# Kernel tuning notes

Hardware: AMD Instinct MI355X
Metric: run time of the kernel (lower is better)

## Reference

```python
import jax, jax.numpy as jnp
import numpy as np

N, L, D_MODEL, NUM_HEADS, MAX_SEQ = 4, 1024, 1024, 16, 2048
DEPTH = D_MODEL // NUM_HEADS


def setup_inputs() -> dict:
    key = jax.random.key(0)
    ks = jax.random.split(key, 12)
    inv = 1.0 / np.sqrt(D_MODEL)
    inp = {
        "q_in": jax.random.normal(ks[0], (N, L, D_MODEL), jnp.float32),
        "k_in": jax.random.normal(ks[1], (N, L, D_MODEL), jnp.float32),
        "v_in": jax.random.normal(ks[2], (N, L, D_MODEL), jnp.float32),
        # causal additive mask: 1.0 where attention is disallowed (j > i)
        "mask": (jnp.triu(jnp.ones((L, L), jnp.float32), k=1))[None, None, :, :],
        "Wq": jax.random.normal(ks[3], (D_MODEL, D_MODEL), jnp.float32) * inv,
        "bq": jnp.zeros((D_MODEL,), jnp.float32),
        "Wk": jax.random.normal(ks[4], (D_MODEL, D_MODEL), jnp.float32) * inv,
        "bk": jnp.zeros((D_MODEL,), jnp.float32),
        "Wv": jax.random.normal(ks[5], (D_MODEL, D_MODEL), jnp.float32) * inv,
        "bv": jnp.zeros((D_MODEL,), jnp.float32),
        "Wo": jax.random.normal(ks[6], (D_MODEL, D_MODEL), jnp.float32) * inv,
        "bo": jnp.zeros((D_MODEL,), jnp.float32),
        "pos_emb": jax.random.normal(ks[7], (MAX_SEQ, DEPTH), jnp.float32) * 0.02,
    }
    return inp


def _rel_bias(q, pos_emb):
    """q: [N,H,L,depth] -> skewed relative-position bias s: [N,H,L,L]."""
    n, h, l, d = q.shape
    e = pos_emb[pos_emb.shape[0] - l:, :]                     # [L, depth]
    qe = jnp.einsum('nhld,md->nhlm', q, e)                    # [N,H,L,L]
    # keep only the last (i+1) entries of row i (upper-left triangle zeroed)
    m = qe.shape[-1]
    keep = (jnp.arange(m)[None, :] >= (m - 1 - jnp.arange(l))[:, None]).astype(qe.dtype)
    qe = qe * keep
    # skew via pad/reshape/slice
    padded = jnp.pad(qe, ((0, 0), (0, 0), (0, 0), (1, 0)))    # [N,H,L,L+1]
    s = padded.reshape(n, h, l + 1, l)[:, :, 1:, :]           # [N,H,L,L]
    return s


def reference(q_in, k_in, v_in, mask, Wq, bq, Wk, bk, Wv, bv, Wo, bo, pos_emb):
    n, l, dm = q_in.shape
    h, d = NUM_HEADS, DEPTH

    def split(x):
        return x.reshape(n, l, h, d).transpose(0, 2, 1, 3)    # [N,H,L,depth]

    q = split(q_in @ Wq + bq)
    k = split(k_in @ Wk + bk)
    v = split(v_in @ Wv + bv)

    s = _rel_bias(q, pos_emb)
    logits = (jnp.einsum('nhld,nhmd->nhlm', q, k) + s) / jnp.sqrt(jnp.float32(d))
    logits = logits + mask * (-1e9)
    attn = jax.nn.softmax(logits, axis=-1)                    # [N,H,L,L]
    out = jnp.einsum('nhlm,nhmd->nhld', attn, v)
    out = out.transpose(0, 2, 1, 3).reshape(n, l, dm)
    return out @ Wo + bo
```

## Files before the change

kernel.cpp:

```cpp
#include <hip/hip_runtime.h>

typedef unsigned short u16t;
typedef unsigned int   u32t;
typedef __bf16 bf16x8 __attribute__((ext_vector_type(8)));
typedef float  f32x4  __attribute__((ext_vector_type(4)));

#define NB     4
#define SEQ    1024
#define DMODEL 1024
#define NHEAD  16
#define DEPTH  64
#define MAXSEQ 2048
#define MTOK   (NB * SEQ)

#define AS1 __attribute__((address_space(1)))
#define AS3 __attribute__((address_space(3)))

__device__ __forceinline__ u16t f2bf(float f) {
  u32t u = __builtin_bit_cast(u32t, f);
  u32t r = (u + 0x7fffu + ((u >> 16) & 1u)) >> 16;
  return (u16t)r;
}
__device__ __forceinline__ float bf2f(u16t h) {
  return __builtin_bit_cast(float, (u32t)h << 16);
}
__device__ __forceinline__ void load_lds16(const void* g, void* l) {
  __builtin_amdgcn_global_load_lds((AS1 u32t*)(g), (AS3 u32t*)(l), 16, 0, 0);
}
__device__ __forceinline__ bf16x8 pack8(f32x4 a, f32x4 b) {
  bf16x8 r;
  r[0] = (__bf16)a[0]; r[1] = (__bf16)a[1]; r[2] = (__bf16)a[2]; r[3] = (__bf16)a[3];
  r[4] = (__bf16)b[0]; r[5] = (__bf16)b[1]; r[6] = (__bf16)b[2]; r[7] = (__bf16)b[3];
  return r;
}

__global__ void transpose4_kernel(const float* __restrict__ w0, const float* __restrict__ w1,
                                  const float* __restrict__ w2, const float* __restrict__ w3,
                                  u16t* __restrict__ t0, u16t* __restrict__ t1,
                                  u16t* __restrict__ t2, u16t* __restrict__ t3,
                                  const float* __restrict__ pe, u16t* __restrict__ Er) {
  const int z = blockIdx.z;
  if (z == 4) {
    const int flat = blockIdx.y * 32 + blockIdx.x;
    if (flat < 256) {
      const int idx = flat * 256 + threadIdx.x;
      const int r = idx >> 6, d = idx & 63;
      Er[idx] = f2bf(pe[(size_t)(MAXSEQ - 1 - r) * DEPTH + d]);
    }
    return;
  }
  const float* W = (z == 0) ? w0 : ((z == 1) ? w1 : ((z == 2) ? w2 : w3));
  u16t* WT = (z == 0) ? t0 : ((z == 1) ? t1 : ((z == 2) ? t2 : t3));
  __shared__ float tile[32][33];
  const int tx = threadIdx.x & 31, ty = threadIdx.x >> 5;
  const int bx = blockIdx.x * 32, by = blockIdx.y * 32;
#pragma unroll
  for (int r = 0; r < 32; r += 8)
    tile[ty + r][tx] = W[(size_t)(by + ty + r) * DMODEL + bx + tx];
  __syncthreads();
#pragma unroll
  for (int r = 0; r < 32; r += 8)
    WT[(size_t)(bx + ty + r) * DMODEL + by + tx] = f2bf(tile[tx][ty + r]);
}

__device__ __forceinline__ void gemm_qkv_body(
    const float* __restrict__ A32, const u16t* __restrict__ BT,
    const float* __restrict__ bias, u16t* __restrict__ C,
    int M, int Nc, int K, int bx, int by, float scale) {
  __shared__ __align__(16) u16t As[128 * 32];
  __shared__ __align__(16) u16t Bs[128 * 32];
  const int tid = threadIdx.x;
  const int wave = tid >> 6;
  const int lane = tid & 63;
  const int q = lane >> 4, t = lane & 15;
  const int lrow = lane >> 2, lch = lane & 3;
  const int bm = by * 128, bn = bx * 128;
  const int wi = (wave >> 1) * 64, wj = (wave & 1) * 64;

  f32x4 acc[4][4];
#pragma unroll
  for (int i = 0; i < 4; ++i)
#pragma unroll
    for (int j = 0; j < 4; ++j) acc[i][j] = f32x4{0.f, 0.f, 0.f, 0.f};

  for (int kt = 0; kt < K; kt += 32) {
    __syncthreads();
    {
      const int rb0 = wave * 16, rb1 = 64 + wave * 16;
      const u16t* gb0 = BT + (size_t)(bn + rb0 + lrow) * K + kt + lch * 8;
      const u16t* gb1 = BT + (size_t)(bn + rb1 + lrow) * K + kt + lch * 8;
      load_lds16(gb0, Bs + rb0 * 32);
      load_lds16(gb1, Bs + rb1 * 32);
      const float* ga0 = A32 + (size_t)(bm + rb0 + lrow) * K + kt + lch * 8;
      const float* ga1 = A32 + (size_t)(bm + rb1 + lrow) * K + kt + lch * 8;
      f32x4 a00 = *(const f32x4*)ga0, a01 = *(const f32x4*)(ga0 + 4);
      f32x4 a10 = *(const f32x4*)ga1, a11 = *(const f32x4*)(ga1 + 4);
      *(bf16x8*)(As + (rb0 + lrow) * 32 + lch * 8) = pack8(a00, a01);
      *(bf16x8*)(As + (rb1 + lrow) * 32 + lch * 8) = pack8(a10, a11);
    }
    __syncthreads();
    bf16x8 af[4], bfr[4];
#pragma unroll
    for (int i = 0; i < 4; ++i) {
      af[i]  = *(const bf16x8*)(As + (wi + i * 16 + t) * 32 + q * 8);
      bfr[i] = *(const bf16x8*)(Bs + (wj + i * 16 + t) * 32 + q * 8);
    }
#pragma unroll
    for (int i = 0; i < 4; ++i)
#pragma unroll
      for (int j = 0; j < 4; ++j)
        acc[i][j] = __builtin_amdgcn_mfma_f32_16x16x32_bf16(af[i], bfr[j], acc[i][j], 0, 0, 0);
  }
#pragma unroll
  for (int j = 0; j < 4; ++j) {
    const int col = bn + wj + j * 16 + t;
    const float bv = bias[col];
#pragma unroll
    for (int i = 0; i < 4; ++i) {
#pragma unroll
      for (int r = 0; r < 4; ++r) {
        const int row = bm + wi + i * 16 + q * 4 + r;
        C[(size_t)row * Nc + col] = f2bf((acc[i][j][r] + bv) * scale);
      }
    }
  }
}

__global__ __launch_bounds__(256, 3) void gemm_qkv_kernel(
    const float* qa, const float* ka, const float* va,
    const u16t* wq, const u16t* wk, const u16t* wv,
    const float* bq, const float* bk, const float* bv,
    u16t* qo, u16t* ko, u16t* vo) {
  const int z = blockIdx.z;
  const float* A = (z == 0) ? qa : ((z == 1) ? ka : va);
  const u16t* B = (z == 0) ? wq : ((z == 1) ? wk : wv);
  const float* bb = (z == 0) ? bq : ((z == 1) ? bk : bv);
  u16t* C = (z == 0) ? qo : ((z == 1) ? ko : vo);
  const float scale = (z == 0) ? 0.125f : 1.0f;
  gemm_qkv_body(A, B, bb, C, MTOK, DMODEL, DMODEL, blockIdx.x, blockIdx.y, scale);
}

__global__ __launch_bounds__(512) void gemm_out_kernel(
    const u16t* __restrict__ A, const u16t* __restrict__ W,
    const float* __restrict__ bias, float* __restrict__ C) {
  __shared__ __align__(16) u16t As[128 * 32];
  __shared__ __align__(16) u16t Bs[128 * 32];
  const int tid = threadIdx.x;
  const int wave = tid >> 6, lane = tid & 63;
  const int q = lane >> 4, t = lane & 15;
  const int srow = wave * 16 + (lane >> 2);
  const int sch = (lane & 3) * 8;
  const int bm = blockIdx.y * 128, bn = blockIdx.x * 128;
  const int wi = (wave >> 1) * 32, wj = (wave & 1) * 64;
  const int K = DMODEL, Nc = DMODEL;

  f32x4 acc[2][4];
#pragma unroll
  for (int i = 0; i < 2; ++i)
#pragma unroll
    for (int j = 0; j < 4; ++j) acc[i][j] = f32x4{0.f, 0.f, 0.f, 0.f};

  for (int kt = 0; kt < K; kt += 32) {
    __syncthreads();
    load_lds16(A + (size_t)(bm + srow) * K + kt + sch, As + wave * 16 * 32);
    load_lds16(W + (size_t)(bn + srow) * K + kt + sch, Bs + wave * 16 * 32);
    __syncthreads();
    bf16x8 af[2], bfr[4];
#pragma unroll
    for (int i = 0; i < 2; ++i)
      af[i] = *(const bf16x8*)(As + (wi + i * 16 + t) * 32 + q * 8);
#pragma unroll
    for (int j = 0; j < 4; ++j)
      bfr[j] = *(const bf16x8*)(Bs + (wj + j * 16 + t) * 32 + q * 8);
#pragma unroll
    for (int i = 0; i < 2; ++i)
#pragma unroll
      for (int j = 0; j < 4; ++j)
        acc[i][j] = __builtin_amdgcn_mfma_f32_16x16x32_bf16(af[i], bfr[j], acc[i][j], 0, 0, 0);
  }
#pragma unroll
  for (int j = 0; j < 4; ++j) {
    const int col = bn + wj + j * 16 + t;
    const float bv = bias[col];
#pragma unroll
    for (int i = 0; i < 2; ++i) {
#pragma unroll
      for (int r = 0; r < 4; ++r) {
        const int row = bm + wi + i * 16 + q * 4 + r;
        C[(size_t)row * Nc + col] = acc[i][j][r] + bv;
      }
    }
  }
}

__global__ __launch_bounds__(512, 4) void attn_kernel(
    const u16t* __restrict__ Qp, const u16t* __restrict__ Kp,
    const u16t* __restrict__ Vp, const u16t* __restrict__ Er,
    u16t* __restrict__ AO) {
  const int gx = blockIdx.x;
  const int xcd = gx & 7, slot = gx >> 3;
  const int ghi = slot & 7, k4 = slot >> 3;
  const int T = (k4 < 4) ? (7 - k4) : (k4 - 4);
  const int g = (ghi << 3) | xcd;
  const int n = g >> 4, h = g & 15;

  const int tid = threadIdx.x;
  const int wave = tid >> 6, lane = tid & 63;
  const int q = lane >> 4, t = lane & 15;
  const int rr = tid >> 3;
  const int c0 = (tid & 7) * 8;

  __shared__ __align__(16) u16t Es[256 * 72];
  __shared__ __align__(16) u16t Ks[64 * 72];
  __shared__ __align__(16) u16t Vt[64 * 64];
  __shared__ __align__(16) u16t TP[8 * 1152];
  u16t* TPw = TP + wave * 1152;

  const int I0 = T * 128;
  const int iw = I0 + wave * 16;
  const int jmax = 2 * T + 1;

  const size_t qoff = ((size_t)(n * SEQ + iw + t)) * DMODEL + h * DEPTH;
  const bf16x8 qf0 = *(const bf16x8*)(Qp + qoff + q * 8);
  const bf16x8 qf1 = *(const bf16x8*)(Qp + qoff + 32 + q * 8);

  const uint4 epre0 = *(const uint4*)(Er + ((size_t)(2 * T) * 64 + rr) * DEPTH + c0);
  const uint4 epre1 = *(const uint4*)(Er + ((size_t)(2 * T + 1) * 64 + rr) * DEPTH + c0);
  const size_t kvoff0 = ((size_t)(n * SEQ + rr)) * DMODEL + h * DEPTH + c0;
  uint4 kv = *(const uint4*)(Kp + kvoff0);
  uint4 vv = *(const uint4*)(Vp + kvoff0);
  uint4 ev = *(const uint4*)(Er + ((ptrdiff_t)(2 * T - 1) * 64 + rr) * DEPTH + c0);

  *(uint4*)(Es + (((2 * T) & 3) * 64 + rr) * 72 + c0) = epre0;
  *(uint4*)(Es + (((2 * T + 1) & 3) * 64 + rr) * 72 + c0) = epre1;

  f32x4 o[4];
#pragma unroll
  for (int c = 0; c < 4; ++c) o[c] = f32x4{0.f, 0.f, 0.f, 0.f};
  float l_r[4] = {0.f, 0.f, 0.f, 0.f};

  for (int jt = 0; jt <= jmax; ++jt) {
    const int J0 = jt * 64;
    const int cnew = 2 * T - 1 - jt;

    __syncthreads();
    *(uint4*)(Ks + rr * 72 + c0) = kv;
    *(uint4*)(Es + ((cnew & 3) * 64 + rr) * 72 + c0) = ev;
    {
      const u16t* pv = (const u16t*)&vv;
#pragma unroll
      for (int uu = 0; uu < 8; ++uu) {
        const int d = c0 + uu;
        Vt[d * 64 + (rr ^ (((d >> 2) & 7) << 3))] = pv[uu];
      }
    }
    __syncthreads();

    if (jt < jmax) {
      const size_t kvoff = ((size_t)(n * SEQ + J0 + 64 + rr)) * DMODEL + h * DEPTH + c0;
      kv = *(const uint4*)(Kp + kvoff);
      vv = *(const uint4*)(Vp + kvoff);
      ev = *(const uint4*)(Er + ((ptrdiff_t)(cnew - 1) * 64 + rr) * DEPTH + c0);
    }

    __builtin_amdgcn_s_setprio(1);
    f32x4 s[4];
#pragma unroll
    for (int c = 0; c < 4; ++c) s[c] = f32x4{0.f, 0.f, 0.f, 0.f};
#pragma unroll
    for (int kk = 0; kk < 2; ++kk) {
      const bf16x8 qf = kk ? qf1 : qf0;
#pragma unroll
      for (int c = 0; c < 4; ++c) {
        const bf16x8 kf = *(const bf16x8*)(Ks + (c * 16 + t) * 72 + kk * 32 + q * 8);
        s[c] = __builtin_amdgcn_mfma_f32_16x16x32_bf16(qf, kf, s[c], 0, 0, 0);
      }
    }
    const int D0 = iw - J0 - 63;
    f32x4 tb[5];
#pragma unroll
    for (int cc = 0; cc < 5; ++cc) tb[cc] = f32x4{0.f, 0.f, 0.f, 0.f};
#pragma unroll
    for (int kk = 0; kk < 2; ++kk) {
      const bf16x8 qf = kk ? qf1 : qf0;
#pragma unroll
      for (int cc = 0; cc < 5; ++cc) {
        const int sl = (int)(((unsigned)(D0 + cc * 16 + t)) & 255u);
        const bf16x8 ef = *(const bf16x8*)(Es + sl * 72 + kk * 32 + q * 8);
        tb[cc] = __builtin_amdgcn_mfma_f32_16x16x32_bf16(qf, ef, tb[cc], 0, 0, 0);
      }
    }
    __builtin_amdgcn_s_setprio(0);
#pragma unroll
    for (int cc = 0; cc < 5; ++cc)
#pragma unroll
      for (int r = 0; r < 4; ++r) {
        const int kp = cc * 16 + t - q * 4 - r;
        if ((unsigned)kp < 64u)
          TPw[(q * 4 + r) * 72 + kp] = f2bf(tb[cc][r]);
      }

    const int dIJ = I0 - J0;
#pragma unroll
    for (int c = 0; c < 4; ++c) {
      const int jc = c * 16 + t;
#pragma unroll
      for (int r = 0; r < 4; ++r) {
        const int ic = wave * 16 + q * 4 + r;
        float lg = s[c][r] + bf2f(TPw[(q * 4 + r) * 72 + 63 - c * 16 - t]);
        lg = (jc <= ic + dIJ) ? lg : -1e30f;
        const float pr = __expf(lg);
        s[c][r] = pr;
        l_r[r] += pr;
      }
    }
#pragma unroll
    for (int c = 0; c < 4; ++c)
#pragma unroll
      for (int r = 0; r < 4; ++r)
        TPw[(q * 4 + r) * 72 + c * 16 + t] = f2bf(s[c][r]);

    const bf16x8 pf0 = *(const bf16x8*)(TPw + t * 72 + q * 8);
    const bf16x8 pf1 = *(const bf16x8*)(TPw + t * 72 + 32 + q * 8);
    __builtin_amdgcn_s_setprio(1);
#pragma unroll
    for (int c2 = 0; c2 < 4; ++c2) {
      const int dd = c2 * 16 + t;
      const int sw = (dd >> 2) & 7;
      const bf16x8 v0 = *(const bf16x8*)(Vt + dd * 64 + ((0 + q) ^ sw) * 8);
      const bf16x8 v1 = *(const bf16x8*)(Vt + dd * 64 + ((4 + q) ^ sw) * 8);
      o[c2] = __builtin_amdgcn_mfma_f32_16x16x32_bf16(pf0, v0, o[c2], 0, 0, 0);
      o[c2] = __builtin_amdgcn_mfma_f32_16x16x32_bf16(pf1, v1, o[c2], 0, 0, 0);
    }
    __builtin_amdgcn_s_setprio(0);
  }

#pragma unroll
  for (int r = 0; r < 4; ++r) {
    float lsum = l_r[r];
    lsum += __shfl_xor(lsum, 1, 64);
    lsum += __shfl_xor(lsum, 2, 64);
    lsum += __shfl_xor(lsum, 4, 64);
    lsum += __shfl_xor(lsum, 8, 64);
    const float inv = 1.f / lsum;
    const size_t obase = ((size_t)(n * SEQ + iw + q * 4 + r)) * DMODEL + h * DEPTH;
#pragma unroll
    for (int c2 = 0; c2 < 4; ++c2)
      AO[obase + c2 * 16 + t] = f2bf(o[c2][r] * inv);
  }
}

extern "C" void kernel_launch(void* const* d_in, const int* in_sizes, int n_in,
                              void* d_out, int out_size, void* d_ws, size_t ws_size,
                              hipStream_t stream) {
  const float* q_in = (const float*)d_in[0];
  const float* k_in = (const float*)d_in[1];
  const float* v_in = (const float*)d_in[2];
  const float* Wq = (const float*)d_in[4];
  const float* bq = (const float*)d_in[5];
  const float* Wk = (const float*)d_in[6];
  const float* bk = (const float*)d_in[7];
  const float* Wv = (const float*)d_in[8];
  const float* bv = (const float*)d_in[9];
  const float* Wo = (const float*)d_in[10];
  const float* bo = (const float*)d_in[11];
  const float* pe = (const float*)d_in[12];
  float* out = (float*)d_out;

  char* ws = (char*)d_ws;
  constexpr size_t MB = 1ull << 20;
  u16t* Qp  = (u16t*)(ws + 24 * MB);
  u16t* Kp  = (u16t*)(ws + 32 * MB);
  u16t* Vp  = (u16t*)(ws + 40 * MB);
  u16t* AOb = (u16t*)(ws + 48 * MB);
  u16t* WqT = (u16t*)(ws + 56 * MB);
  u16t* WkT = (u16t*)(ws + 58 * MB);
  u16t* WvT = (u16t*)(ws + 60 * MB);
  u16t* WoT = (u16t*)(ws + 62 * MB);
  u16t* Erl = (u16t*)(ws + 64 * MB + 16 * 1024);

  transpose4_kernel<<<dim3(32, 32, 5), 256, 0, stream>>>(Wq, Wk, Wv, Wo, WqT, WkT, WvT, WoT,
                                                         pe, Erl);

  gemm_qkv_kernel<<<dim3(DMODEL / 128, MTOK / 128, 3), 256, 0, stream>>>(
      q_in, k_in, v_in, WqT, WkT, WvT, bq, bk, bv, Qp, Kp, Vp);

  attn_kernel<<<dim3(512, 1, 1), 512, 0, stream>>>(Qp, Kp, Vp, Erl, AOb);

  gemm_out_kernel<<<dim3(DMODEL / 128, MTOK / 128, 1), 512, 0, stream>>>(AOb, WoT, bo, out);
}
```

Baseline: 253.1 us.

## Pre-convert QKV inputs to bf16 and remap GEMM blocks across XCDs

Adds a separate kernel that converts the three fp32 activation inputs to bf16 up front, so the QKV projection GEMM can stage both operands into LDS with direct global-to-LDS loads instead of doing register loads and packing in the inner loop. It also remaps block indices in the QKV and output GEMMs so that blocks sharing operand tiles land on the same XCD, aiming for better L2 reuse. The trade-off is an extra pass that reads 48MB of fp32 and writes 24MB of bf16, plus one more kernel launch.

```diff
diff --git a/kernel.cpp b/kernel.cpp
--- a/kernel.cpp
+++ b/kernel.cpp
@@ -27,11 +27,20 @@
 __device__ __forceinline__ void load_lds16(const void* g, void* l) {
   __builtin_amdgcn_global_load_lds((AS1 u32t*)(g), (AS3 u32t*)(l), 16, 0, 0);
 }
-__device__ __forceinline__ bf16x8 pack8(f32x4 a, f32x4 b) {
-  bf16x8 r;
-  r[0] = (__bf16)a[0]; r[1] = (__bf16)a[1]; r[2] = (__bf16)a[2]; r[3] = (__bf16)a[3];
-  r[4] = (__bf16)b[0]; r[5] = (__bf16)b[1]; r[6] = (__bf16)b[2]; r[7] = (__bf16)b[3];
-  return r;
+
+__global__ void cvt3_kernel(const float* __restrict__ a, const float* __restrict__ b,
+                            const float* __restrict__ c,
+                            u16t* __restrict__ oa, u16t* __restrict__ ob,
+                            u16t* __restrict__ oc, int n8) {
+  int i = blockIdx.x * blockDim.x + threadIdx.x;
+  if (i >= n8) return;
+  const float* src = (blockIdx.z == 0) ? a : ((blockIdx.z == 1) ? b : c);
+  u16t* dst = (blockIdx.z == 0) ? oa : ((blockIdx.z == 1) ? ob : oc);
+  const float4* s4 = (const float4*)src;
+  float4 x = s4[2 * i], y = s4[2 * i + 1];
+  u16t tmp[8] = { f2bf(x.x), f2bf(x.y), f2bf(x.z), f2bf(x.w),
+                  f2bf(y.x), f2bf(y.y), f2bf(y.z), f2bf(y.w) };
+  ((uint4*)dst)[i] = *(const uint4*)tmp;
 }
 
 __global__ void transpose4_kernel(const float* __restrict__ w0, const float* __restrict__ w1,
@@ -63,9 +72,17 @@
     WT[(size_t)(bx + ty + r) * DMODEL + by + tx] = f2bf(tile[tx][ty + r]);
 }
 
-__device__ __forceinline__ void gemm_qkv_body(
-    const float* __restrict__ A32, const u16t* __restrict__ BT,
-    const float* __restrict__ bias, u16t* __restrict__ C,
+__device__ __forceinline__ void xcd_remap(int& bx, int& by) {
+  const int flat = blockIdx.x + 8 * blockIdx.y;
+  const int xv = flat & 7, pos = flat >> 3;
+  bx = pos & 7;
+  by = xv * 4 + (pos >> 3);
+}
+
+template <typename OutT>
+__device__ __forceinline__ void gemm_bt_body(
+    const u16t* __restrict__ A, const u16t* __restrict__ BT,
+    const float* __restrict__ bias, OutT* __restrict__ C,
     int M, int Nc, int K, int bx, int by, float scale) {
   __shared__ __align__(16) u16t As[128 * 32];
   __shared__ __align__(16) u16t Bs[128 * 32];
@@ -85,18 +102,13 @@
 
   for (int kt = 0; kt < K; kt += 32) {
     __syncthreads();
-    {
-      const int rb0 = wave * 16, rb1 = 64 + wave * 16;
-      const u16t* gb0 = BT + (size_t)(bn + rb0 + lrow) * K + kt + lch * 8;
-      const u16t* gb1 = BT + (size_t)(bn + rb1 + lrow) * K + kt + lch * 8;
-      load_lds16(gb0, Bs + rb0 * 32);
-      load_lds16(gb1, Bs + rb1 * 32);
-      const float* ga0 = A32 + (size_t)(bm + rb0 + lrow) * K + kt + lch * 8;
-      const float* ga1 = A32 + (size_t)(bm + rb1 + lrow) * K + kt + lch * 8;
-      f32x4 a00 = *(const f32x4*)ga0, a01 = *(const f32x4*)(ga0 + 4);
-      f32x4 a10 = *(const f32x4*)ga1, a11 = *(const f32x4*)(ga1 + 4);
-      *(bf16x8*)(As + (rb0 + lrow) * 32 + lch * 8) = pack8(a00, a01);
-      *(bf16x8*)(As + (rb1 + lrow) * 32 + lch * 8) = pack8(a10, a11);
+#pragma unroll
+    for (int it = 0; it < 2; ++it) {
+      const int rb = it * 64 + wave * 16;
+      const u16t* ga = A + (size_t)(bm + rb + lrow) * K + kt + lch * 8;
+      const u16t* gb = BT + (size_t)(bn + rb + lrow) * K + kt + lch * 8;
+      load_lds16(ga, As + rb * 32);
+      load_lds16(gb, Bs + rb * 32);
     }
     __syncthreads();
     bf16x8 af[4], bfr[4];
@@ -120,24 +132,31 @@
 #pragma unroll
       for (int r = 0; r < 4; ++r) {
         const int row = bm + wi + i * 16 + q * 4 + r;
-        C[(size_t)row * Nc + col] = f2bf((acc[i][j][r] + bv) * scale);
+        float v = (acc[i][j][r] + bv) * scale;
+        if constexpr (sizeof(OutT) == 2) {
+          C[(size_t)row * Nc + col] = f2bf(v);
+        } else {
+          C[(size_t)row * Nc + col] = v;
+        }
       }
     }
   }
 }
 
 __global__ __launch_bounds__(256, 3) void gemm_qkv_kernel(
-    const float* qa, const float* ka, const float* va,
+    const u16t* qa, const u16t* ka, const u16t* va,
     const u16t* wq, const u16t* wk, const u16t* wv,
     const float* bq, const float* bk, const float* bv,
     u16t* qo, u16t* ko, u16t* vo) {
   const int z = blockIdx.z;
-  const float* A = (z == 0) ? qa : ((z == 1) ? ka : va);
+  const u16t* A = (z == 0) ? qa : ((z == 1) ? ka : va);
   const u16t* B = (z == 0) ? wq : ((z == 1) ? wk : wv);
   const float* bb = (z == 0) ? bq : ((z == 1) ? bk : bv);
   u16t* C = (z == 0) ? qo : ((z == 1) ? ko : vo);
   const float scale = (z == 0) ? 0.125f : 1.0f;
-  gemm_qkv_body(A, B, bb, C, MTOK, DMODEL, DMODEL, blockIdx.x, blockIdx.y, scale);
+  int bx, by;
+  xcd_remap(bx, by);
+  gemm_bt_body<u16t>(A, B, bb, C, MTOK, DMODEL, DMODEL, bx, by, scale);
 }
 
 __global__ __launch_bounds__(512) void gemm_out_kernel(
@@ -150,7 +169,9 @@
   const int q = lane >> 4, t = lane & 15;
   const int srow = wave * 16 + (lane >> 2);
   const int sch = (lane & 3) * 8;
-  const int bm = blockIdx.y * 128, bn = blockIdx.x * 128;
+  int bx, by;
+  xcd_remap(bx, by);
+  const int bm = by * 128, bn = bx * 128;
   const int wi = (wave >> 1) * 32, wj = (wave & 1) * 64;
   const int K = DMODEL, Nc = DMODEL;
 
@@ -369,6 +390,9 @@
 
   char* ws = (char*)d_ws;
   constexpr size_t MB = 1ull << 20;
+  u16t* qb  = (u16t*)(ws);
+  u16t* kb  = (u16t*)(ws + 8 * MB);
+  u16t* vb  = (u16t*)(ws + 16 * MB);
   u16t* Qp  = (u16t*)(ws + 24 * MB);
   u16t* Kp  = (u16t*)(ws + 32 * MB);
   u16t* Vp  = (u16t*)(ws + 40 * MB);
@@ -379,11 +403,14 @@
   u16t* WoT = (u16t*)(ws + 62 * MB);
   u16t* Erl = (u16t*)(ws + 64 * MB + 16 * 1024);
 
+  const size_t SZA = (size_t)MTOK * DMODEL;
+  const int n8 = (int)(SZA / 8);
+  cvt3_kernel<<<dim3(n8 / 256, 1, 3), 256, 0, stream>>>(q_in, k_in, v_in, qb, kb, vb, n8);
   transpose4_kernel<<<dim3(32, 32, 5), 256, 0, stream>>>(Wq, Wk, Wv, Wo, WqT, WkT, WvT, WoT,
                                                          pe, Erl);
 
   gemm_qkv_kernel<<<dim3(DMODEL / 128, MTOK / 128, 3), 256, 0, stream>>>(
-      q_in, k_in, v_in, WqT, WkT, WvT, bq, bk, bv, Qp, Kp, Vp);
+      qb, kb, vb, WqT, WkT, WvT, bq, bk, bv, Qp, Kp, Vp);
 
   attn_kernel<<<dim3(512, 1, 1), 512, 0, stream>>>(Qp, Kp, Vp, Erl, AOb);
 
```

Result: faster. 237.4 us (-6.2%).
